# Performance work log

Hardware: AMD Instinct MI355X
Metric: run time of the kernel (lower is better)

The kernel has to match this reference:

```python
import jax, jax.numpy as jnp
import numpy as np

B, T, D = 4, 4096, 1024

def setup_inputs() -> dict:
    key = jax.random.key(0)
    kx, kq, kk, kv = jax.random.split(key, 4)
    s = 1.0 / np.sqrt(D)
    return {
        "x": jax.random.normal(kx, (B, T, D), dtype=jnp.float32),
        "Wq": jax.random.normal(kq, (D, D), dtype=jnp.float32) * s,
        "Wk": jax.random.normal(kk, (D, D), dtype=jnp.float32) * s,
        "Wv": jax.random.normal(kv, (D, D), dtype=jnp.float32) * s,
    }

def reference(x, Wq, Wk, Wv):
    # x: [B, T, D]; W*: [D, D] (torch Linear weight, y = x @ W.T)
    Q = jnp.einsum("btd,ed->bte", x, Wq)
    K = jnp.einsum("btd,ed->bte", x, Wk)
    V = jnp.einsum("btd,ed->bte", x, Wv)
    scale = jnp.asarray(np.sqrt(D), dtype=x.dtype)
    scores = jnp.einsum("bqd,bkd->bqk", Q, K) / scale  # [B, T, T]
    weights = jax.nn.softmax(scores, axis=-1)
    return jnp.einsum("bqk,bkd->bqd", weights, V)
```

## Files before the change

kernel.cpp:

```cpp
#include <hip/hip_runtime.h>
#include <stdint.h>

typedef unsigned short u16;
typedef __attribute__((ext_vector_type(4))) float f32x4;
typedef __attribute__((ext_vector_type(8))) short s16x8;

#define TB 4
#define TT 4096
#define TD 1024

__device__ __forceinline__ u16 f2bf(float f) {
  union { float f; uint32_t u; } v; v.f = f;
  return (u16)((v.u + 0x7FFFu + ((v.u >> 16) & 1u)) >> 16);
}
__device__ __forceinline__ float bf2f(u16 h) {
  union { uint32_t u; float f; } v; v.u = ((uint32_t)h) << 16;
  return v.f;
}

#define GLOAD_LDS16(g, l) __builtin_amdgcn_global_load_lds( \
    (const __attribute__((address_space(1))) void*)(g),      \
    (__attribute__((address_space(3))) void*)(l), 16, 0, 0)

#define MFMA16(a, b, c) __builtin_amdgcn_mfma_f32_16x16x32_bf16(a, b, c, 0, 0, 0)
#define LDSV(o) (*(const s16x8*)&ls[(o)])

__global__ void cast_all(const float* __restrict__ x, const float* __restrict__ wq,
                         const float* __restrict__ wk, const float* __restrict__ wv,
                         u16* __restrict__ dst) {
  const int NX = 1 << 22;
  const int NW = 1 << 18;
  const int NT = NX + 3 * NW;
  int i = blockIdx.x * blockDim.x + threadIdx.x;
  int stride = gridDim.x * blockDim.x;
  for (; i < NT; i += stride) {
    float4 v;
    if (i < NX) {
      v = ((const float4*)x)[i];
    } else {
      int j = i - NX;
      int w = j >> 18;
      int off = j & (NW - 1);
      const float* p = (w == 0) ? wq : (w == 1) ? wk : wv;
      v = ((const float4*)p)[off];
    }
    ushort4 o;
    o.x = f2bf(v.x); o.y = f2bf(v.y); o.z = f2bf(v.z); o.w = f2bf(v.w);
    ((ushort4*)dst)[i] = o;
  }
}

template<bool OUT_BF16>
__global__ __launch_bounds__(512)
void gemm256(const u16* __restrict__ Abase, const u16* __restrict__ Bt,
             void* __restrict__ C, int K, int lda, int ldb, int ldc, float scale,
             size_t oA0, size_t oA1, size_t oA2, size_t oA3,
             size_t sB, size_t sC) {
  __shared__ u16 ls[65536];
  const int tid  = threadIdx.x;
  const int lane = tid & 63;
  const int wid  = tid >> 6;
  const int wm   = wid >> 2;
  const int wn   = wid & 3;

  const int nxy = gridDim.x * gridDim.y;
  const int id  = blockIdx.y * gridDim.x + blockIdx.x;
  const int sid = (id & 7) * (nxy >> 3) + (id >> 3);
  const int bx  = sid % gridDim.x;
  const int by  = sid / gridDim.x;
  const int brow = by * 256;
  const int bcol = bx * 256;

  const int z = blockIdx.z;
  const size_t oA = (z == 0) ? oA0 : (z == 1) ? oA1 : (z == 2) ? oA2 : oA3;
  const u16* A = Abase + oA;
  Bt += (size_t)z * sB;

  const int lr = lane >> 3;
  const int lc = (lane & 7) ^ lr;

  auto STAGE_BLK = [&](int slotB, int kt, int op, int r0) {
    const u16* g = op ? (Bt + (size_t)bcol * ldb) : (A + (size_t)brow * lda);
    const int ld = op ? ldb : lda;
    const int r  = r0 + wid * 8 + lr;
    GLOAD_LDS16(g + (size_t)r * ld + (size_t)kt * 64 + (size_t)lc * 8,
                &ls[slotB + op * 16384 + (r0 + wid * 8) * 64]);
  };

  f32x4 acc[8][4];
#pragma unroll
  for (int m = 0; m < 8; ++m)
#pragma unroll
    for (int n = 0; n < 4; ++n) acc[m][n] = (f32x4){0.f, 0.f, 0.f, 0.f};

  const int nt = K >> 6;

  STAGE_BLK(0, 0, 0, 0);   STAGE_BLK(0, 0, 0, 64);
  STAGE_BLK(0, 0, 0, 128); STAGE_BLK(0, 0, 0, 192);
  STAGE_BLK(0, 0, 1, 0);   STAGE_BLK(0, 0, 1, 64);
  STAGE_BLK(0, 0, 1, 128); STAGE_BLK(0, 0, 1, 192);
  if (nt > 1) {
    STAGE_BLK(32768, 1, 1, 0);   STAGE_BLK(32768, 1, 1, 64);
    STAGE_BLK(32768, 1, 1, 128); STAGE_BLK(32768, 1, 1, 192);
    STAGE_BLK(32768, 1, 0, 0);   STAGE_BLK(32768, 1, 0, 128);
    asm volatile("s_waitcnt vmcnt(6)" ::: "memory");
  } else {
    asm volatile("s_waitcnt vmcnt(0)" ::: "memory");
  }
  __builtin_amdgcn_s_barrier();

  const int r16 = lane & 15;
  const int k8  = lane >> 4;
  const int sw  = r16 & 7;
  const int c0  = ((k8)     ^ sw) * 8;
  const int c1  = ((4 | k8) ^ sw) * 8;
  int aBase[8], bBase[4];
#pragma unroll
  for (int m = 0; m < 8; ++m) aBase[m] = (wm * 128 + m * 16 + r16) * 64;
#pragma unroll
  for (int n = 0; n < 4; ++n) bBase[n] = 16384 + (wn * 64 + n * 16 + r16) * 64;

#define READ_A(P)                                                              \
  af[0][0] = LDSV(sb + aBase[2*(P)]   + c0); af[0][1] = LDSV(sb + aBase[2*(P)]   + c1); \
  af[1][0] = LDSV(sb + aBase[2*(P)+1] + c0); af[1][1] = LDSV(sb + aBase[2*(P)+1] + c1);

#define MIDSYNC()                                                              \
  __builtin_amdgcn_sched_barrier(0);                                           \
  __builtin_amdgcn_s_barrier();                                                \
  asm volatile("s_waitcnt lgkmcnt(0)" ::: "memory");                           \
  __builtin_amdgcn_sched_barrier(0);

#define PHASE_MFMA(P)                                                          \
  __builtin_amdgcn_s_setprio(1);                                               \
  _Pragma("unroll")                                                            \
  for (int mm = 0; mm < 2; ++mm)                                               \
    _Pragma("unroll")                                                          \
    for (int n = 0; n < 4; ++n) {                                              \
      acc[2*(P)+mm][n] = MFMA16(af[mm][0], bf[n][0], acc[2*(P)+mm][n]);        \
      acc[2*(P)+mm][n] = MFMA16(af[mm][1], bf[n][1], acc[2*(P)+mm][n]);        \
    }                                                                          \
  __builtin_amdgcn_s_setprio(0);

  for (int t = 0; t < nt; ++t) {
    const int sb  = (t & 1) << 15;
    const int sbn = sb ^ 32768;
    const bool pf1 = (t + 1 < nt);
    const bool pf2 = (t + 2 < nt);
    s16x8 bf[4][2], af[2][2];

    READ_A(0);
#pragma unroll
    for (int n = 0; n < 4; ++n) {
      bf[n][0] = LDSV(sb + bBase[n] + c0);
      bf[n][1] = LDSV(sb + bBase[n] + c1);
    }
    if (pf1) { STAGE_BLK(sbn, t + 1, 0, 64); STAGE_BLK(sbn, t + 1, 0, 192); }
    MIDSYNC();
    PHASE_MFMA(0);
    __builtin_amdgcn_s_barrier();

    READ_A(1);
    if (pf2) { STAGE_BLK(sb, t + 2, 1, 0); STAGE_BLK(sb, t + 2, 1, 64); }
    MIDSYNC();
    PHASE_MFMA(1);
    __builtin_amdgcn_s_barrier();

    READ_A(2);
    if (pf2) { STAGE_BLK(sb, t + 2, 1, 128); STAGE_BLK(sb, t + 2, 1, 192); }
    MIDSYNC();
    PHASE_MFMA(2);
    __builtin_amdgcn_s_barrier();

    READ_A(3);
    if (pf2) { STAGE_BLK(sb, t + 2, 0, 0); STAGE_BLK(sb, t + 2, 0, 128); }
    MIDSYNC();
    PHASE_MFMA(3);
    if (pf2) asm volatile("s_waitcnt vmcnt(6)" ::: "memory");
    else     asm volatile("s_waitcnt vmcnt(0)" ::: "memory");
    __builtin_amdgcn_sched_barrier(0);
    __builtin_amdgcn_s_barrier();
  }
#undef READ_A
#undef MIDSYNC
#undef PHASE_MFMA

  const int c16 = lane & 15;
  const int rhi = lane >> 4;
#pragma unroll
  for (int m = 0; m < 8; ++m)
#pragma unroll
    for (int n = 0; n < 4; ++n)
#pragma unroll
      for (int r = 0; r < 4; ++r) {
        int grow = brow + wm * 128 + m * 16 + rhi * 4 + r;
        int gcol = bcol + wn * 64 + n * 16 + c16;
        float v = acc[m][n][r] * scale;
        if (OUT_BF16) ((u16*)C)[(size_t)z * sC + (size_t)grow * ldc + gcol] = f2bf(v);
        else          ((float*)C)[(size_t)z * sC + (size_t)grow * ldc + gcol] = v;
      }
}

__global__ __launch_bounds__(256)
void transpose_bf16(const u16* __restrict__ V, u16* __restrict__ Vt) {
  __shared__ u16 tile[64][65];
  int b  = blockIdx.z;
  int t0 = blockIdx.y * 64;
  int e0 = blockIdx.x * 64;
  const u16* Vb  = V  + (size_t)b * TT * TD;
  u16*       Vtb = Vt + (size_t)b * TT * TD;
  int r  = threadIdx.x >> 4;
  int c4 = threadIdx.x & 15;
#pragma unroll
  for (int i = 0; i < 4; ++i) {
    int row = r + i * 16;
    ushort4 v = *(const ushort4*)&Vb[(size_t)(t0 + row) * TD + e0 + c4 * 4];
    tile[row][c4 * 4 + 0] = v.x;
    tile[row][c4 * 4 + 1] = v.y;
    tile[row][c4 * 4 + 2] = v.z;
    tile[row][c4 * 4 + 3] = v.w;
  }
  __syncthreads();
#pragma unroll
  for (int i = 0; i < 4; ++i) {
    int e = r + i * 16;
    ushort4 o;
    o.x = tile[c4 * 4 + 0][e];
    o.y = tile[c4 * 4 + 1][e];
    o.z = tile[c4 * 4 + 2][e];
    o.w = tile[c4 * 4 + 3][e];
    *(ushort4*)&Vtb[(size_t)(e0 + e) * TT + t0 + c4 * 4] = o;
  }
}

__global__ __launch_bounds__(256)
void softmax_bf16(const u16* __restrict__ S, u16* __restrict__ P) {
  __shared__ float red_m[4];
  __shared__ float red_s[4];
  int row  = blockIdx.x;
  int tid  = threadIdx.x;
  int lane = tid & 63;
  int wid  = tid >> 6;
  const s16x8* Sr = (const s16x8*)(S + (size_t)row * 4096);

  float v[16];
  float m = -1e30f;
#pragma unroll
  for (int i = 0; i < 2; ++i) {
    s16x8 u = Sr[tid + i * 256];
#pragma unroll
    for (int j = 0; j < 8; ++j) {
      v[i * 8 + j] = bf2f((u16)u[j]);
      m = fmaxf(m, v[i * 8 + j]);
    }
  }
#pragma unroll
  for (int off = 32; off >= 1; off >>= 1) m = fmaxf(m, __shfl_xor(m, off));
  if (lane == 0) red_m[wid] = m;
  __syncthreads();
  m = fmaxf(fmaxf(red_m[0], red_m[1]), fmaxf(red_m[2], red_m[3]));

  float s = 0.f;
#pragma unroll
  for (int j = 0; j < 16; ++j) { v[j] = __expf(v[j] - m); s += v[j]; }
#pragma unroll
  for (int off = 32; off >= 1; off >>= 1) s += __shfl_xor(s, off);
  if (lane == 0) red_s[wid] = s;
  __syncthreads();
  s = red_s[0] + red_s[1] + red_s[2] + red_s[3];
  float inv = 1.0f / s;

  s16x8* Pr = (s16x8*)(P + (size_t)row * 4096);
#pragma unroll
  for (int i = 0; i < 2; ++i) {
    s16x8 o;
#pragma unroll
    for (int j = 0; j < 8; ++j) o[j] = (short)f2bf(v[i * 8 + j] * inv);
    Pr[tid + i * 256] = o;
  }
}

extern "C" void kernel_launch(void* const* d_in, const int* in_sizes, int n_in,
                              void* d_out, int out_size, void* d_ws, size_t ws_size,
                              hipStream_t stream) {
  const float* x  = (const float*)d_in[0];
  const float* Wq = (const float*)d_in[1];
  const float* Wk = (const float*)d_in[2];
  const float* Wv = (const float*)d_in[3];
  float* out = (float*)d_out;

  const size_t MT = (size_t)TB * TT;
  const size_t BE = (size_t)TT * TD;
  const size_t XE = MT * TD;
  const size_t WE = (size_t)TD * TD;

  u16* xb   = (u16*)d_ws;
  u16* wqb  = xb + XE;
  u16* wkb  = wqb + WE;
  u16* wvb  = wkb + WE;
  u16* Q    = wvb + WE;
  u16* Kb   = Q + XE;
  u16* Vt   = Kb + XE;
  u16* PB   = Vt + XE;
  u16* tmpS = PB + 2 * XE;

  cast_all<<<2048, 256, 0, stream>>>(x, Wq, Wk, Wv, xb);

  dim3 blk(512);
  gemm256<true><<<dim3(TD / 256, MT / 256, 1), blk, 0, stream>>>(
      xb, wqb, Q, TD, TD, TD, TD, 0.03125f, 0, 0, 0, 0, 0, 0);
  gemm256<true><<<dim3(TD / 256, MT / 256, 2), blk, 0, stream>>>(
      xb, wkb, Kb, TD, TD, TD, TD, 1.0f, 0, 0, 0, 0, WE, 2 * XE);

  transpose_bf16<<<dim3(TD / 64, TT / 64, TB), 256, 0, stream>>>(PB, Vt);

  u16* Pp[4] = {xb, PB, PB + XE, Q};
  for (int b = 0; b < TB; ++b) {
    gemm256<true><<<dim3(TT / 256, TT / 256, 1), blk, 0, stream>>>(
        Q + b * BE, Kb + b * BE, tmpS, TD, TD, TD, TT, 1.0f, 0, 0, 0, 0, 0, 0);
    softmax_bf16<<<TT, 256, 0, stream>>>(tmpS, Pp[b]);
  }

  gemm256<false><<<dim3(TD / 256, TT / 256, TB), blk, 0, stream>>>(
      xb, Vt, out, TT, TT, TT, TD, 1.0f,
      0, (size_t)(PB - xb), (size_t)(PB + XE - xb), (size_t)(Q - xb), BE, BE);
}
```

Before: 463.1 us.

## Batch QKV and score GEMMs, in-place batched softmax, register-pipelined LDS reads

The QKV projections now run as one 3-slice launch, and the per-batch score GEMM plus softmax loop becomes a single 4-slice GEMM followed by one in-place softmax over all rows. This removes many small launches and lets each launch fill the whole GPU instead of one batch at a time. Inside the GEMM, the A fragments are double-buffered in registers and the next tile's LDS reads are issued before the barrier. This drops the per-phase lgkmcnt wait and overlaps LDS reads with MFMA work. In exchange it raises register pressure and loosens the ordering of LDS reads against waits, which risks hazards or spills.

```diff
diff --git a/kernel.cpp b/kernel.cpp
--- a/kernel.cpp
+++ b/kernel.cpp
@@ -53,9 +53,10 @@
 template<bool OUT_BF16>
 __global__ __launch_bounds__(512)
 void gemm256(const u16* __restrict__ Abase, const u16* __restrict__ Bt,
-             void* __restrict__ C, int K, int lda, int ldb, int ldc, float scale,
-             size_t oA0, size_t oA1, size_t oA2, size_t oA3,
-             size_t sB, size_t sC) {
+             void* __restrict__ C, int K, int lda, int ldb, int ldc,
+             float s0, float s1,
+             size_t oA0, size_t oA1, size_t oA2, size_t oA3, size_t sB,
+             size_t oC0, size_t oC1, size_t oC2, size_t oC3) {
   __shared__ u16 ls[65536];
   const int tid  = threadIdx.x;
   const int lane = tid & 63;
@@ -73,6 +74,8 @@
 
   const int z = blockIdx.z;
   const size_t oA = (z == 0) ? oA0 : (z == 1) ? oA1 : (z == 2) ? oA2 : oA3;
+  const size_t oC = (z == 0) ? oC0 : (z == 1) ? oC1 : (z == 2) ? oC2 : oC3;
+  const float scale = (z == 0) ? s0 : s1;
   const u16* A = Abase + oA;
   Bt += (size_t)z * sB;
 
@@ -120,69 +123,66 @@
 #pragma unroll
   for (int n = 0; n < 4; ++n) bBase[n] = 16384 + (wn * 64 + n * 16 + r16) * 64;
 
-#define READ_A(P)                                                              \
-  af[0][0] = LDSV(sb + aBase[2*(P)]   + c0); af[0][1] = LDSV(sb + aBase[2*(P)]   + c1); \
-  af[1][0] = LDSV(sb + aBase[2*(P)+1] + c0); af[1][1] = LDSV(sb + aBase[2*(P)+1] + c1);
-
-#define MIDSYNC()                                                              \
-  __builtin_amdgcn_sched_barrier(0);                                           \
-  __builtin_amdgcn_s_barrier();                                                \
-  asm volatile("s_waitcnt lgkmcnt(0)" ::: "memory");                           \
-  __builtin_amdgcn_sched_barrier(0);
-
-#define PHASE_MFMA(P)                                                          \
-  __builtin_amdgcn_s_setprio(1);                                               \
-  _Pragma("unroll")                                                            \
-  for (int mm = 0; mm < 2; ++mm)                                               \
-    _Pragma("unroll")                                                          \
-    for (int n = 0; n < 4; ++n) {                                              \
-      acc[2*(P)+mm][n] = MFMA16(af[mm][0], bf[n][0], acc[2*(P)+mm][n]);        \
-      acc[2*(P)+mm][n] = MFMA16(af[mm][1], bf[n][1], acc[2*(P)+mm][n]);        \
-    }                                                                          \
+  s16x8 bf[4][2], af_x[2][2], af_y[2][2];
+
+#define READ_APAIR(DST, SB, M0)                               \
+  DST[0][0] = LDSV((SB) + aBase[M0] + c0);                    \
+  DST[0][1] = LDSV((SB) + aBase[M0] + c1);                    \
+  DST[1][0] = LDSV((SB) + aBase[(M0) + 1] + c0);              \
+  DST[1][1] = LDSV((SB) + aBase[(M0) + 1] + c1);
+
+#define READ_B(SB)                                            \
+  _Pragma("unroll")                                           \
+  for (int n = 0; n < 4; ++n) {                               \
+    bf[n][0] = LDSV((SB) + bBase[n] + c0);                    \
+    bf[n][1] = LDSV((SB) + bBase[n] + c1);                    \
+  }
+
+#define CLUSTER(MB, AF)                                                  \
+  __builtin_amdgcn_s_setprio(1);                                         \
+  _Pragma("unroll")                                                      \
+  for (int mm = 0; mm < 2; ++mm)                                         \
+    _Pragma("unroll")                                                    \
+    for (int n = 0; n < 4; ++n) {                                        \
+      acc[(MB) + mm][n] = MFMA16(AF[mm][0], bf[n][0], acc[(MB) + mm][n]); \
+      acc[(MB) + mm][n] = MFMA16(AF[mm][1], bf[n][1], acc[(MB) + mm][n]); \
+    }                                                                    \
   __builtin_amdgcn_s_setprio(0);
+
+  READ_B(0);
+  READ_APAIR(af_x, 0, 0);
 
   for (int t = 0; t < nt; ++t) {
     const int sb  = (t & 1) << 15;
     const int sbn = sb ^ 32768;
     const bool pf1 = (t + 1 < nt);
     const bool pf2 = (t + 2 < nt);
-    s16x8 bf[4][2], af[2][2];
-
-    READ_A(0);
-#pragma unroll
-    for (int n = 0; n < 4; ++n) {
-      bf[n][0] = LDSV(sb + bBase[n] + c0);
-      bf[n][1] = LDSV(sb + bBase[n] + c1);
-    }
+
     if (pf1) { STAGE_BLK(sbn, t + 1, 0, 64); STAGE_BLK(sbn, t + 1, 0, 192); }
-    MIDSYNC();
-    PHASE_MFMA(0);
+    READ_APAIR(af_y, sb, 2);
+    CLUSTER(0, af_x);
     __builtin_amdgcn_s_barrier();
 
-    READ_A(1);
     if (pf2) { STAGE_BLK(sb, t + 2, 1, 0); STAGE_BLK(sb, t + 2, 1, 64); }
-    MIDSYNC();
-    PHASE_MFMA(1);
+    READ_APAIR(af_x, sb, 4);
+    CLUSTER(2, af_y);
     __builtin_amdgcn_s_barrier();
 
-    READ_A(2);
     if (pf2) { STAGE_BLK(sb, t + 2, 1, 128); STAGE_BLK(sb, t + 2, 1, 192); }
-    MIDSYNC();
-    PHASE_MFMA(2);
+    READ_APAIR(af_y, sb, 6);
+    CLUSTER(4, af_x);
+    if (pf2) asm volatile("s_waitcnt vmcnt(4)" ::: "memory");
+    else     asm volatile("s_waitcnt vmcnt(0)" ::: "memory");
     __builtin_amdgcn_s_barrier();
 
-    READ_A(3);
     if (pf2) { STAGE_BLK(sb, t + 2, 0, 0); STAGE_BLK(sb, t + 2, 0, 128); }
-    MIDSYNC();
-    PHASE_MFMA(3);
-    if (pf2) asm volatile("s_waitcnt vmcnt(6)" ::: "memory");
-    else     asm volatile("s_waitcnt vmcnt(0)" ::: "memory");
-    __builtin_amdgcn_sched_barrier(0);
+    CLUSTER(6, af_y);
+    if (pf1) { READ_B(sbn); READ_APAIR(af_x, sbn, 0); }
     __builtin_amdgcn_s_barrier();
   }
-#undef READ_A
-#undef MIDSYNC
-#undef PHASE_MFMA
+#undef READ_APAIR
+#undef READ_B
+#undef CLUSTER
 
   const int c16 = lane & 15;
   const int rhi = lane >> 4;
@@ -195,8 +195,8 @@
         int grow = brow + wm * 128 + m * 16 + rhi * 4 + r;
         int gcol = bcol + wn * 64 + n * 16 + c16;
         float v = acc[m][n][r] * scale;
-        if (OUT_BF16) ((u16*)C)[(size_t)z * sC + (size_t)grow * ldc + gcol] = f2bf(v);
-        else          ((float*)C)[(size_t)z * sC + (size_t)grow * ldc + gcol] = v;
+        if (OUT_BF16) ((u16*)C)[oC + (size_t)grow * ldc + gcol] = f2bf(v);
+        else          ((float*)C)[oC + (size_t)grow * ldc + gcol] = v;
       }
 }
 
@@ -233,14 +233,17 @@
 }
 
 __global__ __launch_bounds__(256)
-void softmax_bf16(const u16* __restrict__ S, u16* __restrict__ P) {
+void softmax4(u16* __restrict__ p0, u16* __restrict__ p1,
+              u16* __restrict__ p2, u16* __restrict__ p3) {
   __shared__ float red_m[4];
   __shared__ float red_s[4];
-  int row  = blockIdx.x;
+  const int bi = blockIdx.x >> 12;
+  u16* base = (bi == 0) ? p0 : (bi == 1) ? p1 : (bi == 2) ? p2 : p3;
+  const int row = blockIdx.x & 4095;
   int tid  = threadIdx.x;
   int lane = tid & 63;
   int wid  = tid >> 6;
-  const s16x8* Sr = (const s16x8*)(S + (size_t)row * 4096);
+  s16x8* Sr = (s16x8*)(base + (size_t)row * 4096);
 
   float v[16];
   float m = -1e30f;
@@ -269,13 +272,12 @@
   s = red_s[0] + red_s[1] + red_s[2] + red_s[3];
   float inv = 1.0f / s;
 
-  s16x8* Pr = (s16x8*)(P + (size_t)row * 4096);
 #pragma unroll
   for (int i = 0; i < 2; ++i) {
     s16x8 o;
 #pragma unroll
     for (int j = 0; j < 8; ++j) o[j] = (short)f2bf(v[i * 8 + j] * inv);
-    Pr[tid + i * 256] = o;
+    Sr[tid + i * 256] = o;
   }
 }
 
@@ -295,9 +297,7 @@
 
   u16* xb   = (u16*)d_ws;
   u16* wqb  = xb + XE;
-  u16* wkb  = wqb + WE;
-  u16* wvb  = wkb + WE;
-  u16* Q    = wvb + WE;
+  u16* Q    = wqb + 3 * WE;
   u16* Kb   = Q + XE;
   u16* Vt   = Kb + XE;
   u16* PB   = Vt + XE;
@@ -306,21 +306,22 @@
   cast_all<<<2048, 256, 0, stream>>>(x, Wq, Wk, Wv, xb);
 
   dim3 blk(512);
-  gemm256<true><<<dim3(TD / 256, MT / 256, 1), blk, 0, stream>>>(
-      xb, wqb, Q, TD, TD, TD, TD, 0.03125f, 0, 0, 0, 0, 0, 0);
-  gemm256<true><<<dim3(TD / 256, MT / 256, 2), blk, 0, stream>>>(
-      xb, wkb, Kb, TD, TD, TD, TD, 1.0f, 0, 0, 0, 0, WE, 2 * XE);
+  gemm256<true><<<dim3(TD / 256, MT / 256, 3), blk, 0, stream>>>(
+      xb, wqb, Q, TD, TD, TD, TD, 0.03125f, 1.0f,
+      0, 0, 0, 0, WE,
+      0, XE, (size_t)(PB - Q), 0);
 
   transpose_bf16<<<dim3(TD / 64, TT / 64, TB), 256, 0, stream>>>(PB, Vt);
 
-  u16* Pp[4] = {xb, PB, PB + XE, Q};
-  for (int b = 0; b < TB; ++b) {
-    gemm256<true><<<dim3(TT / 256, TT / 256, 1), blk, 0, stream>>>(
-        Q + b * BE, Kb + b * BE, tmpS, TD, TD, TD, TT, 1.0f, 0, 0, 0, 0, 0, 0);
-    softmax_bf16<<<TT, 256, 0, stream>>>(tmpS, Pp[b]);
-  }
+  gemm256<true><<<dim3(TT / 256, TT / 256, TB), blk, 0, stream>>>(
+      Q, Kb, xb, TD, TD, TD, TT, 1.0f, 1.0f,
+      0, BE, 2 * BE, 3 * BE, BE,
+      0, (size_t)(PB - xb), (size_t)(PB + XE - xb), (size_t)(tmpS - xb));
+
+  softmax4<<<dim3(TB * TT), 256, 0, stream>>>(xb, PB, PB + XE, tmpS);
 
   gemm256<false><<<dim3(TD / 256, TT / 256, TB), blk, 0, stream>>>(
-      xb, Vt, out, TT, TT, TT, TD, 1.0f,
-      0, (size_t)(PB - xb), (size_t)(PB + XE - xb), (size_t)(Q - xb), BE, BE);
-}
+      xb, Vt, out, TT, TT, TT, TD, 1.0f, 1.0f,
+      0, (size_t)(PB - xb), (size_t)(PB + XE - xb), (size_t)(tmpS - xb), BE,
+      0, BE, 2 * BE, 3 * BE);
+}
```

New measurement: 438.8 us. 5.2% less time.
